# Kernel tuning notes

Hardware: AMD Instinct MI355X
Metric: run time of the kernel (lower is better)

## Reference

```python
import jax, jax.numpy as jnp
import numpy as np

N_NODES = 100_000
N_EDGES = 1_600_000
F_IN, F_HID, F_OUT = 128, 64, 128


def setup_inputs() -> dict:
    key = jax.random.key(0)
    k_x, k_e, k_w1, k_w2 = jax.random.split(key, 4)
    x = jax.random.normal(k_x, (N_NODES, F_IN), dtype=jnp.float32)
    edge_index = jax.random.randint(k_e, (2, N_EDGES), 0, N_NODES, dtype=jnp.int32)
    # Glorot-style init for the two GCN conv weight matrices
    W1 = jax.random.normal(k_w1, (F_IN, F_HID), dtype=jnp.float32) * (1.0 / np.sqrt(F_IN))
    b1 = jnp.zeros((F_HID,), dtype=jnp.float32)
    W2 = jax.random.normal(k_w2, (F_HID, F_OUT), dtype=jnp.float32) * (1.0 / np.sqrt(F_HID))
    b2 = jnp.zeros((F_OUT,), dtype=jnp.float32)
    return {"x": x, "edge_index": edge_index, "W1": W1, "b1": b1, "W2": W2, "b2": b2}


def _gcn_conv(x, W, b, src, dst, num_nodes):
    """GCNConv: out = D^{-1/2} (A + I) D^{-1/2} (x W) + b.
    Self-loops handled analytically: deg includes +1, and the self-loop
    message for node i is norm_i^2 * h_i."""
    h = x @ W  # [N, F_out]
    ones = jnp.ones(src.shape[0], dtype=h.dtype)
    deg = jax.ops.segment_sum(ones, dst, num_segments=num_nodes) + 1.0  # +1 self-loop
    norm = jax.lax.rsqrt(deg)  # [N]
    # gather source messages scaled by norm_src, scatter-add into dst
    agg = jax.ops.segment_sum(h[src] * norm[src, None], dst, num_segments=num_nodes)
    return norm[:, None] * agg + (norm * norm)[:, None] * h + b


def reference(x, edge_index, W1, b1, W2, b2):
    src, dst = edge_index[0], edge_index[1]
    n = x.shape[0]
    h = jax.nn.relu(_gcn_conv(x, W1, b1, src, dst, n))
    # dropout p=0.0 -> identity (module default)
    return _gcn_conv(h, W2, b2, src, dst, n)
```

## Files before the change

kernel.cpp:

```cpp
#include <hip/hip_runtime.h>
#include <hip/hip_bf16.h>

#define F_IN 128
#define F_HID 64
#define F_OUT 128
#define BSH 9
#define BS  (1 << BSH)
#define MAXNB 256

__device__ __forceinline__ int clampi(int v, int lo, int hi) {
    return v < lo ? lo : (v > hi ? hi : v);
}

__device__ __forceinline__ unsigned short f2bf(float f) {
    unsigned int u = __float_as_uint(f);
    u = (u + 0x7FFFu + ((u >> 16) & 1u)) >> 16;
    return (unsigned short)u;
}
__device__ __forceinline__ float bf2f(unsigned short s) {
    return __uint_as_float(((unsigned int)s) << 16);
}

__global__ void zero2_kernel(int* __restrict__ a, int* __restrict__ b, int n) {
    int i = blockIdx.x * blockDim.x + threadIdx.x;
    if (i < n) { a[i] = 0; b[i] = 0; }
}

__global__ void bhist_kernel(const int* __restrict__ dst, int* __restrict__ bhist,
                             int E, int Nn, int NB) {
    __shared__ int lh[MAXNB];
    for (int i = threadIdx.x; i < NB; i += 256) lh[i] = 0;
    __syncthreads();
    int chunk = (E + gridDim.x - 1) / gridDim.x;
    int base = blockIdx.x * chunk;
    int end = base + chunk; if (end > E) end = E;
    for (int i = base + threadIdx.x; i < end; i += 256) {
        int d = clampi(dst[i], 0, Nn - 1);
        atomicAdd(&lh[d >> BSH], 1);
    }
    __syncthreads();
    for (int i = threadIdx.x; i < NB; i += 256)
        if (lh[i]) atomicAdd(&bhist[i], lh[i]);
}

__global__ void bplace_kernel(const int* __restrict__ src, const int* __restrict__ dst,
                              const int* __restrict__ bhist, int* __restrict__ bbase,
                              int* __restrict__ bcur,
                              int* __restrict__ staging, int E, int Nn, int NB) {
    __shared__ int lh[MAXNB];
    __shared__ int gb[MAXNB];
    __shared__ int bb[MAXNB];
    int t = threadIdx.x;
    int v = (t < NB) ? bhist[t] : 0;
    bb[t] = v;
    __syncthreads();
    for (int d = 1; d < MAXNB; d <<= 1) {
        int x = (t >= d) ? bb[t - d] : 0;
        __syncthreads();
        bb[t] += x;
        __syncthreads();
    }
    int excl = bb[t] - v;
    __syncthreads();
    bb[t] = excl;
    if (blockIdx.x == 0 && t < NB) bbase[t] = excl;
    for (int i = t; i < NB; i += 256) lh[i] = 0;
    __syncthreads();

    int chunk = (E + gridDim.x - 1) / gridDim.x;
    int base = blockIdx.x * chunk;
    int end = base + chunk; if (end > E) end = E;
    for (int i = base + t; i < end; i += 256) {
        int d = clampi(dst[i], 0, Nn - 1);
        atomicAdd(&lh[d >> BSH], 1);
    }
    __syncthreads();
    for (int i = t; i < NB; i += 256) {
        int c = lh[i];
        gb[i] = (c > 0) ? bb[i] + atomicAdd(&bcur[i], c) : 0;
        lh[i] = 0;
    }
    __syncthreads();
    for (int i = base + t; i < end; i += 256) {
        int d = clampi(dst[i], 0, Nn - 1);
        int s = clampi(src[i], 0, Nn - 1);
        int b = d >> BSH;
        int p = gb[b] + atomicAdd(&lh[b], 1);
        staging[p] = (s << BSH) | (d & (BS - 1));
    }
}

__global__ void bfine_kernel(const int* __restrict__ bhist, const int* __restrict__ bbase,
                             const int* __restrict__ staging,
                             int* __restrict__ cnt, int* __restrict__ off,
                             float* __restrict__ nrm, int* __restrict__ csr, int Nn) {
    __shared__ int lcnt[BS];
    __shared__ int loff[BS];
    __shared__ int lcur[BS];
    __shared__ int ps[256];
    int b = blockIdx.x;
    int t = threadIdx.x;
    int base  = bbase[b];
    int count = bhist[b];
    int node0 = b << BSH;

    for (int r = t; r < BS; r += 256) lcnt[r] = 0;
    __syncthreads();
    for (int i = t; i < count; i += 256)
        atomicAdd(&lcnt[staging[base + i] & (BS - 1)], 1);
    __syncthreads();

    int a0 = lcnt[2 * t], a1 = lcnt[2 * t + 1];
    int pair = a0 + a1;
    ps[t] = pair;
    __syncthreads();
    for (int d = 1; d < 256; d <<= 1) {
        int x = (t >= d) ? ps[t - d] : 0;
        __syncthreads();
        ps[t] += x;
        __syncthreads();
    }
    int excl = ps[t] - pair;
    loff[2 * t]     = excl;
    loff[2 * t + 1] = excl + a0;
    __syncthreads();

    for (int r = t; r < BS; r += 256) {
        int node = node0 + r;
        if (node < Nn) {
            int c = lcnt[r];
            cnt[node] = c;
            off[node] = base + loff[r];
            nrm[node] = rsqrtf((float)c + 1.0f);
        }
        lcur[r] = 0;
    }
    __syncthreads();

    for (int i = t; i < count; i += 256) {
        int v = staging[base + i];
        int r = v & (BS - 1);
        int p = base + loff[r] + atomicAdd(&lcur[r], 1);
        csr[p] = v >> BSH;
    }
}

template<int K, int N, bool PRESCALE, bool BIAS, bool BF16OUT>
__global__ void gemm_tiled(const float* __restrict__ A, const float* __restrict__ B,
                           const float* __restrict__ nrm, const float* __restrict__ bias,
                           void* __restrict__ Cv, int M) {
    constexpr int CT = N / 8;
    constexpr int RB = (256 / CT) * 4;
    __shared__ float Ws[K * N];

    int tid = threadIdx.x;
    for (int i = tid; i < K * N / 4; i += 256)
        ((float4*)Ws)[i] = ((const float4*)B)[i];
    __syncthreads();

    int ct = tid % CT;
    int rt = tid / CT;
    int row0 = blockIdx.x * RB + rt * 4;
    int c0 = ct * 8;

    float acc[4][8];
#pragma unroll
    for (int r = 0; r < 4; r++)
#pragma unroll
        for (int c = 0; c < 8; c++) acc[r][c] = 0.f;

    for (int kk = 0; kk < K; kk += 8) {
        float4 av[4], av2[4];
#pragma unroll
        for (int r = 0; r < 4; r++) {
            int row = row0 + r;
            if (row < M) {
                av[r]  = *(const float4*)(A + (size_t)row * K + kk);
                av2[r] = *(const float4*)(A + (size_t)row * K + kk + 4);
            } else {
                av[r]  = make_float4(0.f, 0.f, 0.f, 0.f);
                av2[r] = make_float4(0.f, 0.f, 0.f, 0.f);
            }
        }
#pragma unroll
        for (int j = 0; j < 4; j++) {
            const float* wrow = Ws + (kk + j) * N + c0;
            float4 w0 = *(const float4*)(wrow);
            float4 w1 = *(const float4*)(wrow + 4);
            float wj[8] = {w0.x, w0.y, w0.z, w0.w, w1.x, w1.y, w1.z, w1.w};
#pragma unroll
            for (int r = 0; r < 4; r++) {
                float a = (j == 0) ? av[r].x : (j == 1) ? av[r].y : (j == 2) ? av[r].z : av[r].w;
#pragma unroll
                for (int c = 0; c < 8; c++)
                    acc[r][c] = fmaf(a, wj[c], acc[r][c]);
            }
        }
#pragma unroll
        for (int j = 0; j < 4; j++) {
            const float* wrow = Ws + (kk + 4 + j) * N + c0;
            float4 w0 = *(const float4*)(wrow);
            float4 w1 = *(const float4*)(wrow + 4);
            float wj[8] = {w0.x, w0.y, w0.z, w0.w, w1.x, w1.y, w1.z, w1.w};
#pragma unroll
            for (int r = 0; r < 4; r++) {
                float a = (j == 0) ? av2[r].x : (j == 1) ? av2[r].y : (j == 2) ? av2[r].z : av2[r].w;
#pragma unroll
                for (int c = 0; c < 8; c++)
                    acc[r][c] = fmaf(a, wj[c], acc[r][c]);
            }
        }
    }

    float bcol[8];
    if (BIAS) {
        float4 bb0 = *(const float4*)(bias + c0);
        float4 bb1 = *(const float4*)(bias + c0 + 4);
        bcol[0]=bb0.x; bcol[1]=bb0.y; bcol[2]=bb0.z; bcol[3]=bb0.w;
        bcol[4]=bb1.x; bcol[5]=bb1.y; bcol[6]=bb1.z; bcol[7]=bb1.w;
    }

#pragma unroll
    for (int r = 0; r < 4; r++) {
        int row = row0 + r;
        if (row >= M) continue;
        float scale = PRESCALE ? nrm[row] : 1.0f;
        float o[8];
#pragma unroll
        for (int c = 0; c < 8; c++) {
            float v = acc[r][c];
            if (PRESCALE) v *= scale;
            if (BIAS)     v += bcol[c];
            o[c] = v;
        }
        if (BF16OUT) {
            unsigned int pk0 = (unsigned int)f2bf(o[0]) | ((unsigned int)f2bf(o[1]) << 16);
            unsigned int pk1 = (unsigned int)f2bf(o[2]) | ((unsigned int)f2bf(o[3]) << 16);
            unsigned int pk2 = (unsigned int)f2bf(o[4]) | ((unsigned int)f2bf(o[5]) << 16);
            unsigned int pk3 = (unsigned int)f2bf(o[6]) | ((unsigned int)f2bf(o[7]) << 16);
            uint4 pk; pk.x = pk0; pk.y = pk1; pk.z = pk2; pk.w = pk3;
            *(uint4*)((unsigned short*)Cv + (size_t)row * N + c0) = pk;
        } else {
            float4 o0, o1;
            o0.x = o[0]; o0.y = o[1]; o0.z = o[2]; o0.w = o[3];
            o1.x = o[4]; o1.y = o[5]; o1.z = o[6]; o1.w = o[7];
            float* crow = (float*)Cv + (size_t)row * N + c0;
            *(float4*)(crow) = o0;
            *(float4*)(crow + 4) = o1;
        }
    }
}

template<bool CONV>
__global__ void gather64_kernel(const unsigned short* __restrict__ h,
                                const float* __restrict__ norm,
                                const int* __restrict__ off, const int* __restrict__ cnt,
                                const int* __restrict__ csr_src,
                                const float* __restrict__ bias,
                                void* __restrict__ outv, int Nn, int E) {
    int wave = (blockIdx.x * blockDim.x + threadIdx.x) >> 6;
    int lane = threadIdx.x & 63;
    int node = __builtin_amdgcn_readfirstlane(wave);
    if (node >= Nn) return;

    int o0 = __builtin_amdgcn_readfirstlane(off[node]);
    int c  = __builtin_amdgcn_readfirstlane(cnt[node]);
    if (c < 0) c = 0;
    if (o0 < 0) o0 = 0;
    if (o0 + c > E) c = E - o0;

    const int* ce = csr_src + o0;
    float sum = 0.0f;
    int e = 0;
    for (; e + 16 <= c; e += 16) {
        int si[16];
        unsigned short v[16];
#pragma unroll
        for (int u = 0; u < 16; u++) si[u] = clampi(ce[e + u], 0, Nn - 1);
#pragma unroll
        for (int u = 0; u < 16; u++) v[u] = h[(size_t)si[u] * 64 + lane];
#pragma unroll
        for (int u = 0; u < 16; u++) sum += bf2f(v[u]);
    }
    for (; e + 8 <= c; e += 8) {
        int si[8];
        unsigned short v[8];
#pragma unroll
        for (int u = 0; u < 8; u++) si[u] = clampi(ce[e + u], 0, Nn - 1);
#pragma unroll
        for (int u = 0; u < 8; u++) v[u] = h[(size_t)si[u] * 64 + lane];
#pragma unroll
        for (int u = 0; u < 8; u++) sum += bf2f(v[u]);
    }
    for (; e + 4 <= c; e += 4) {
        int si[4];
        unsigned short v[4];
#pragma unroll
        for (int u = 0; u < 4; u++) si[u] = clampi(ce[e + u], 0, Nn - 1);
#pragma unroll
        for (int u = 0; u < 4; u++) v[u] = h[(size_t)si[u] * 64 + lane];
#pragma unroll
        for (int u = 0; u < 4; u++) sum += bf2f(v[u]);
    }
    for (; e < c; e++) {
        int s = clampi(ce[e], 0, Nn - 1);
        sum += bf2f(h[(size_t)s * 64 + lane]);
    }
    float self = bf2f(h[(size_t)node * 64 + lane]);
    float nv = norm[node];
    float r = nv * (sum + self);
    if (CONV) {
        r = nv * fmaxf(r + bias[lane], 0.0f);
        ((unsigned short*)outv)[(size_t)node * 64 + lane] = f2bf(r);
    } else {
        ((float*)outv)[(size_t)node * 64 + lane] = r;
    }
}

extern "C" void kernel_launch(void* const* d_in, const int* in_sizes, int n_in,
                              void* d_out, int out_size, void* d_ws, size_t ws_size,
                              hipStream_t stream) {
    if (n_in < 6) return;
    const float* x   = (const float*)d_in[0];
    const int*   ei  = (const int*)d_in[1];
    const float* W1  = (const float*)d_in[2];
    const float* b1  = (const float*)d_in[3];
    const float* W2  = (const float*)d_in[4];
    const float* b2  = (const float*)d_in[5];
    float*       out = (float*)d_out;

    int Nn = in_sizes[0] / F_IN;
    int E  = in_sizes[1] / 2;
    const int* src = ei;
    const int* dst = ei + E;

    int NB = (Nn + BS - 1) >> BSH;
    if (NB > MAXNB) return;
    if (Nn > (1 << (31 - BSH))) return;

    size_t o = 0;
    auto alloc = [&](size_t bytes) { size_t cur = o; o += (bytes + 255) & ~(size_t)255; return cur; };
    size_t o_cnt   = alloc((size_t)Nn * 4);
    size_t o_off   = alloc((size_t)Nn * 4);
    size_t o_nrm   = alloc((size_t)Nn * 4);
    size_t o_csr   = alloc((size_t)E * 4);
    size_t o_stg   = alloc((size_t)E * 4);
    size_t o_bh    = alloc(MAXNB * 4);
    size_t o_bb    = alloc(MAXNB * 4);
    size_t o_bc    = alloc(MAXNB * 4);
    size_t o_h     = alloc((size_t)Nn * F_HID * 4);
    if (o > ws_size) return;

    char* ws = (char*)d_ws;
    int*   cnt   = (int*)(ws + o_cnt);
    int*   off   = (int*)(ws + o_off);
    float* nrm   = (float*)(ws + o_nrm);
    int*   csr   = (int*)(ws + o_csr);
    int*   stg   = (int*)(ws + o_stg);
    int*   bh    = (int*)(ws + o_bh);
    int*   bb    = (int*)(ws + o_bb);
    int*   bc    = (int*)(ws + o_bc);
    unsigned short* h1 = (unsigned short*)(ws + o_h);
    float*          q  = (float*)(ws + o_h);
    unsigned short* p  = (unsigned short*)(out + (size_t)Nn * F_HID);

    zero2_kernel<<<1, 256, 0, stream>>>(bh, bc, MAXNB);
    bhist_kernel<<<256, 256, 0, stream>>>(dst, bh, E, Nn, NB);
    bplace_kernel<<<256, 256, 0, stream>>>(src, dst, bh, bb, bc, stg, E, Nn, NB);
    bfine_kernel<<<NB, 256, 0, stream>>>(bh, bb, stg, cnt, off, nrm, csr, Nn);

    {
        constexpr int RB = (256 / (F_HID / 8)) * 4;
        gemm_tiled<F_IN, F_HID, true, false, true><<<(Nn + RB - 1) / RB, 256, 0, stream>>>(
            x, W1, nrm, nullptr, h1, Nn);
    }
    gather64_kernel<true><<<(Nn + 3) / 4, 256, 0, stream>>>(
        h1, nrm, off, cnt, csr, b1, p, Nn, E);

    gather64_kernel<false><<<(Nn + 3) / 4, 256, 0, stream>>>(
        p, nrm, off, cnt, csr, nullptr, q, Nn, E);
    {
        constexpr int RB = (256 / (F_OUT / 8)) * 4;
        gemm_tiled<F_HID, F_OUT, false, true, false><<<(Nn + RB - 1) / RB, 256, 0, stream>>>(
            q, W2, nullptr, b2, out, Nn);
    }
}
```

Before: 326.1 us.

## Fuse first GEMM with bucket placement kernel and move norm scaling into gather

The first GEMM no longer depends on the node norms, so it runs in one launch alongside the edge bucket-placement pass. Blocks below NG do the GEMM and the rest do placement, sharing a union of shared memory. The per-source norm scaling moves into the first gather, where each edge now makes an extra norm[src] load. The aim is to overlap the compute-bound GEMM with the atomic-heavy placement and save one launch, at the cost of more random loads per edge in the gather.

```diff
diff --git a/kernel.cpp b/kernel.cpp
--- a/kernel.cpp
+++ b/kernel.cpp
@@ -43,32 +43,30 @@
         if (lh[i]) atomicAdd(&bhist[i], lh[i]);
 }
 
-__global__ void bplace_kernel(const int* __restrict__ src, const int* __restrict__ dst,
-                              const int* __restrict__ bhist, int* __restrict__ bbase,
-                              int* __restrict__ bcur,
-                              int* __restrict__ staging, int E, int Nn, int NB) {
-    __shared__ int lh[MAXNB];
-    __shared__ int gb[MAXNB];
-    __shared__ int bb[MAXNB];
+__device__ void bplace_body(int* lh, int* gb, int* bbuf, int lb, int NPL,
+                            const int* __restrict__ src, const int* __restrict__ dst,
+                            const int* __restrict__ bhist, int* __restrict__ bbase,
+                            int* __restrict__ bcur, int* __restrict__ staging,
+                            int E, int Nn, int NB) {
     int t = threadIdx.x;
     int v = (t < NB) ? bhist[t] : 0;
-    bb[t] = v;
-    __syncthreads();
-    for (int d = 1; d < MAXNB; d <<= 1) {
-        int x = (t >= d) ? bb[t - d] : 0;
+    bbuf[t] = v;
+    __syncthreads();
+    for (int dd = 1; dd < MAXNB; dd <<= 1) {
+        int x = (t >= dd) ? bbuf[t - dd] : 0;
         __syncthreads();
-        bb[t] += x;
+        bbuf[t] += x;
         __syncthreads();
     }
-    int excl = bb[t] - v;
-    __syncthreads();
-    bb[t] = excl;
-    if (blockIdx.x == 0 && t < NB) bbase[t] = excl;
+    int excl = bbuf[t] - v;
+    __syncthreads();
+    bbuf[t] = excl;
+    if (lb == 0 && t < NB) bbase[t] = excl;
     for (int i = t; i < NB; i += 256) lh[i] = 0;
     __syncthreads();
 
-    int chunk = (E + gridDim.x - 1) / gridDim.x;
-    int base = blockIdx.x * chunk;
+    int chunk = (E + NPL - 1) / NPL;
+    int base = lb * chunk;
     int end = base + chunk; if (end > E) end = E;
     for (int i = base + t; i < end; i += 256) {
         int d = clampi(dst[i], 0, Nn - 1);
@@ -77,7 +75,7 @@
     __syncthreads();
     for (int i = t; i < NB; i += 256) {
         int c = lh[i];
-        gb[i] = (c > 0) ? bb[i] + atomicAdd(&bcur[i], c) : 0;
+        gb[i] = (c > 0) ? bbuf[i] + atomicAdd(&bcur[i], c) : 0;
         lh[i] = 0;
     }
     __syncthreads();
@@ -145,13 +143,13 @@
     }
 }
 
-template<int K, int N, bool PRESCALE, bool BIAS, bool BF16OUT>
-__global__ void gemm_tiled(const float* __restrict__ A, const float* __restrict__ B,
-                           const float* __restrict__ nrm, const float* __restrict__ bias,
-                           void* __restrict__ Cv, int M) {
+template<int K, int N, bool BIAS, bool BF16OUT>
+__device__ void gemm_body(float* __restrict__ Ws, int lb,
+                          const float* __restrict__ A, const float* __restrict__ B,
+                          const float* __restrict__ bias,
+                          void* __restrict__ Cv, int M) {
     constexpr int CT = N / 8;
     constexpr int RB = (256 / CT) * 4;
-    __shared__ float Ws[K * N];
 
     int tid = threadIdx.x;
     for (int i = tid; i < K * N / 4; i += 256)
@@ -160,7 +158,7 @@
 
     int ct = tid % CT;
     int rt = tid / CT;
-    int row0 = blockIdx.x * RB + rt * 4;
+    int row0 = lb * RB + rt * 4;
     int c0 = ct * 8;
 
     float acc[4][8];
@@ -224,13 +222,11 @@
     for (int r = 0; r < 4; r++) {
         int row = row0 + r;
         if (row >= M) continue;
-        float scale = PRESCALE ? nrm[row] : 1.0f;
         float o[8];
 #pragma unroll
         for (int c = 0; c < 8; c++) {
             float v = acc[r][c];
-            if (PRESCALE) v *= scale;
-            if (BIAS)     v += bcol[c];
+            if (BIAS) v += bcol[c];
             o[c] = v;
         }
         if (BF16OUT) {
@@ -251,13 +247,107 @@
     }
 }
 
-template<bool CONV>
-__global__ void gather64_kernel(const unsigned short* __restrict__ h,
-                                const float* __restrict__ norm,
-                                const int* __restrict__ off, const int* __restrict__ cnt,
-                                const int* __restrict__ csr_src,
-                                const float* __restrict__ bias,
-                                void* __restrict__ outv, int Nn, int E) {
+template<int K, int N, bool BIAS, bool BF16OUT>
+__global__ void gemm_tiled(const float* __restrict__ A, const float* __restrict__ B,
+                           const float* __restrict__ bias,
+                           void* __restrict__ Cv, int M) {
+    __shared__ float Ws[K * N];
+    gemm_body<K, N, BIAS, BF16OUT>(Ws, blockIdx.x, A, B, bias, Cv, M);
+}
+
+__global__ void gemm1_bplace_kernel(const float* __restrict__ x, const float* __restrict__ W1,
+                                    unsigned short* __restrict__ h1, int M, int NG,
+                                    const int* __restrict__ src, const int* __restrict__ dst,
+                                    const int* __restrict__ bhist, int* __restrict__ bbase,
+                                    int* __restrict__ bcur, int* __restrict__ staging,
+                                    int E, int Nn, int NB, int NPL) {
+    __shared__ union SmA {
+        float ws[F_IN * F_HID];
+        struct { int lh[MAXNB]; int gb[MAXNB]; int bb[MAXNB]; } pl;
+    } sm;
+    if ((int)blockIdx.x < NG) {
+        gemm_body<F_IN, F_HID, false, true>(sm.ws, blockIdx.x, x, W1, nullptr, h1, M);
+    } else {
+        bplace_body(sm.pl.lh, sm.pl.gb, sm.pl.bb, blockIdx.x - NG, NPL,
+                    src, dst, bhist, bbase, bcur, staging, E, Nn, NB);
+    }
+}
+
+__global__ void gather64_conv_kernel(const unsigned short* __restrict__ h,
+                                     const float* __restrict__ norm,
+                                     const int* __restrict__ off, const int* __restrict__ cnt,
+                                     const int* __restrict__ csr_src,
+                                     const float* __restrict__ bias,
+                                     unsigned short* __restrict__ outp, int Nn, int E) {
+    int wave = (blockIdx.x * blockDim.x + threadIdx.x) >> 6;
+    int lane = threadIdx.x & 63;
+    int node = __builtin_amdgcn_readfirstlane(wave);
+    if (node >= Nn) return;
+
+    int o0 = __builtin_amdgcn_readfirstlane(off[node]);
+    int c  = __builtin_amdgcn_readfirstlane(cnt[node]);
+    if (c < 0) c = 0;
+    if (o0 < 0) o0 = 0;
+    if (o0 + c > E) c = E - o0;
+
+    const int* ce = csr_src + o0;
+    float sum = 0.0f;
+    int e = 0;
+    for (; e + 16 <= c; e += 16) {
+        int si[16];
+        float nw[16];
+        unsigned short v[16];
+#pragma unroll
+        for (int u = 0; u < 16; u++) si[u] = clampi(ce[e + u], 0, Nn - 1);
+#pragma unroll
+        for (int u = 0; u < 16; u++) nw[u] = norm[si[u]];
+#pragma unroll
+        for (int u = 0; u < 16; u++) v[u] = h[(size_t)si[u] * 64 + lane];
+#pragma unroll
+        for (int u = 0; u < 16; u++) sum = fmaf(nw[u], bf2f(v[u]), sum);
+    }
+    for (; e + 8 <= c; e += 8) {
+        int si[8];
+        float nw[8];
+        unsigned short v[8];
+#pragma unroll
+        for (int u = 0; u < 8; u++) si[u] = clampi(ce[e + u], 0, Nn - 1);
+#pragma unroll
+        for (int u = 0; u < 8; u++) nw[u] = norm[si[u]];
+#pragma unroll
+        for (int u = 0; u < 8; u++) v[u] = h[(size_t)si[u] * 64 + lane];
+#pragma unroll
+        for (int u = 0; u < 8; u++) sum = fmaf(nw[u], bf2f(v[u]), sum);
+    }
+    for (; e + 4 <= c; e += 4) {
+        int si[4];
+        float nw[4];
+        unsigned short v[4];
+#pragma unroll
+        for (int u = 0; u < 4; u++) si[u] = clampi(ce[e + u], 0, Nn - 1);
+#pragma unroll
+        for (int u = 0; u < 4; u++) nw[u] = norm[si[u]];
+#pragma unroll
+        for (int u = 0; u < 4; u++) v[u] = h[(size_t)si[u] * 64 + lane];
+#pragma unroll
+        for (int u = 0; u < 4; u++) sum = fmaf(nw[u], bf2f(v[u]), sum);
+    }
+    for (; e < c; e++) {
+        int s = clampi(ce[e], 0, Nn - 1);
+        sum = fmaf(norm[s], bf2f(h[(size_t)s * 64 + lane]), sum);
+    }
+    float self = bf2f(h[(size_t)node * 64 + lane]);
+    float nv = norm[node];
+    float r = nv * (sum + nv * self);
+    r = nv * fmaxf(r + bias[lane], 0.0f);
+    outp[(size_t)node * 64 + lane] = f2bf(r);
+}
+
+__global__ void gather64_plain_kernel(const unsigned short* __restrict__ h,
+                                      const float* __restrict__ norm,
+                                      const int* __restrict__ off, const int* __restrict__ cnt,
+                                      const int* __restrict__ csr_src,
+                                      float* __restrict__ outq, int Nn, int E) {
     int wave = (blockIdx.x * blockDim.x + threadIdx.x) >> 6;
     int lane = threadIdx.x & 63;
     int node = __builtin_amdgcn_readfirstlane(wave);
@@ -308,13 +398,7 @@
     }
     float self = bf2f(h[(size_t)node * 64 + lane]);
     float nv = norm[node];
-    float r = nv * (sum + self);
-    if (CONV) {
-        r = nv * fmaxf(r + bias[lane], 0.0f);
-        ((unsigned short*)outv)[(size_t)node * 64 + lane] = f2bf(r);
-    } else {
-        ((float*)outv)[(size_t)node * 64 + lane] = r;
-    }
+    outq[(size_t)node * 64 + lane] = nv * (sum + self);
 }
 
 extern "C" void kernel_launch(void* const* d_in, const int* in_sizes, int n_in,
@@ -366,22 +450,20 @@
 
     zero2_kernel<<<1, 256, 0, stream>>>(bh, bc, MAXNB);
     bhist_kernel<<<256, 256, 0, stream>>>(dst, bh, E, Nn, NB);
-    bplace_kernel<<<256, 256, 0, stream>>>(src, dst, bh, bb, bc, stg, E, Nn, NB);
+    int G1 = (Nn + 127) / 128;
+    gemm1_bplace_kernel<<<G1 + 256, 256, 0, stream>>>(
+        x, W1, h1, Nn, G1,
+        src, dst, bh, bb, bc, stg, E, Nn, NB, 256);
     bfine_kernel<<<NB, 256, 0, stream>>>(bh, bb, stg, cnt, off, nrm, csr, Nn);
 
-    {
-        constexpr int RB = (256 / (F_HID / 8)) * 4;
-        gemm_tiled<F_IN, F_HID, true, false, true><<<(Nn + RB - 1) / RB, 256, 0, stream>>>(
-            x, W1, nrm, nullptr, h1, Nn);
-    }
-    gather64_kernel<true><<<(Nn + 3) / 4, 256, 0, stream>>>(
+    gather64_conv_kernel<<<(Nn + 3) / 4, 256, 0, stream>>>(
         h1, nrm, off, cnt, csr, b1, p, Nn, E);
 
-    gather64_kernel<false><<<(Nn + 3) / 4, 256, 0, stream>>>(
-        p, nrm, off, cnt, csr, nullptr, q, Nn, E);
+    gather64_plain_kernel<<<(Nn + 3) / 4, 256, 0, stream>>>(
+        p, nrm, off, cnt, csr, q, Nn, E);
     {
         constexpr int RB = (256 / (F_OUT / 8)) * 4;
-        gemm_tiled<F_HID, F_OUT, false, true, false><<<(Nn + RB - 1) / RB, 256, 0, stream>>>(
-            q, W2, nullptr, b2, out, Nn);
-    }
-}
+        gemm_tiled<F_HID, F_OUT, true, false><<<(Nn + RB - 1) / RB, 256, 0, stream>>>(
+            q, W2, b2, out, Nn);
+    }
+}
```

Result: no change. 320.6 us (-1.7%).
